# Kernel tuning notes

Hardware: AMD Instinct MI355X
Metric: run time of the kernel (lower is better)

## Reference

```python
import jax, jax.numpy as jnp
import numpy as np

STRIDE = 25
TOPK = 3
EPS = 1e-9


def setup_inputs() -> dict:
    key = jax.random.key(0)
    k1, k2, k3, k4 = jax.random.split(key, 4)
    B, N, T, P = 128, 200, 360, 400
    x = jax.random.normal(k1, (B, N, T), dtype=jnp.float32)
    # per-sample time-series lengths; min 100 so size_after_pool >= 1
    length = jax.random.randint(k2, (B,), 100, T + 1)
    # xavier_uniform with gain=1.414 as in nn.init.xavier_uniform_(.., gain=1.414)
    limit = float(np.sqrt(6.0 / (P + N)) * 1.414)
    patterns = jax.random.uniform(k3, (P, N), minval=-limit, maxval=limit, dtype=jnp.float32)
    # simple linear classifier standing in for Baselines.mlp(num_of_node)
    W_cls = jax.random.normal(k4, (N * N, 2), dtype=jnp.float32) * 0.01
    b_cls = jnp.zeros((2,), dtype=jnp.float32)
    return {"x": x, "length": length, "patterns": patterns, "W_cls": W_cls, "b_cls": b_cls}


def _forward(x, length, patterns, W_cls, b_cls):
    B, N, T = x.shape
    P = patterns.shape[0]
    # size_after_pool = floor(length / stride)  [B]
    sap = (length // STRIDE).astype(jnp.int32)
    # MRI_length_regularize (random_start=False): the scatter-mask keeps
    # t < size_after_pool*stride per sample; padded tail is exactly zero and
    # contributes 0 through maxpool+sum, so static full-T masking is equivalent.
    valid = (jnp.arange(T)[None, :] < (sap * STRIDE)[:, None]).astype(x.dtype)  # [B,T]
    frames = (x * valid[:, None, :]).transpose(0, 2, 1)  # [B,T,N]
    nf = frames / jnp.sqrt((frames ** 2).sum(-1, keepdims=True) + EPS)
    npat = patterns / jnp.sqrt((patterns ** 2).sum(-1, keepdims=True) + EPS)
    # top_select: keep top-K |entries| per pattern row
    _, topi = jax.lax.top_k(jnp.abs(npat), TOPK)  # [P,K]
    pmask = jnp.zeros((P, N), x.dtype).at[jnp.arange(P)[:, None], topi].set(1.0)
    toppattern = pmask * npat
    # scores + strided max-pool over time
    scores = jnp.einsum('btn,pn->bpt', nf, npat)  # [B,P,T]
    nwin = T // STRIDE
    pos = scores[:, :, : nwin * STRIDE].reshape(B, P, nwin, STRIDE).max(-1)  # [B,P,nwin]
    finalscore = (pos / sap[:, None, None].astype(x.dtype)).sum(-1)  # [B,P]
    # realpattern = toppattern.detach(); graphs = R^T diag(finalscore) R / (maskgraph+eps)
    realpattern = jax.lax.stop_gradient(toppattern)
    maskgraph = pmask.T @ pmask  # [N,N]
    graphs = jnp.einsum('pn,bp,pm->bnm', realpattern, finalscore, realpattern) / (maskgraph + EPS)
    out = graphs.reshape(B, -1) @ W_cls + b_cls  # [B,2]
    # Critical_ROI(normalized_patterns, toppattern)
    norm = (((1.0 - jnp.linalg.norm(toppattern, axis=-1) / jnp.linalg.norm(npat, axis=-1)) ** 2).sum() / 800.0)
    rec = jnp.zeros((1,), x.dtype)
    return out, norm, rec


def reference(x, length, patterns, W_cls, b_cls):
    return _forward(x, length, patterns, W_cls, b_cls)
```

## Files before the change

kernel.cpp:

```cpp
#include <hip/hip_runtime.h>

#define N_NODE 200
#define T_LEN 360
#define T_POOL 350
#define P_PAT 400
#define P_PAD 512
#define NWIN 14
#define STRIDE_ 25
#define KPAD 224

#define O_AH    0
#define O_POS   229376
#define O_TOPN  3899392
#define O_TOPV  3904192
#define O_NORMT 3908992

typedef unsigned short u16;
typedef __attribute__((ext_vector_type(8))) short bf16x8;
typedef __attribute__((ext_vector_type(4))) float f32x4;

#define RP 2064
#define DBS 8256
#define SQOFF 16512
#define IVOFF 18560
#define SMEM_BYTES 19072

__device__ __forceinline__ unsigned fkey(float f) {
    unsigned u = __float_as_uint(f);
    return (u & 0x80000000u) ? ~u : (u | 0x80000000u);
}
__device__ __forceinline__ u16 f2bf(float f) {
    unsigned u = __float_as_uint(f);
    unsigned r = u + 0x7FFFu + ((u >> 16) & 1u);
    return (u16)(r >> 16);
}

__global__ void k_pat(const float* __restrict__ pat, u16* __restrict__ Ah,
                      int* __restrict__ topn_w, float* __restrict__ topv_w,
                      float* __restrict__ normt, unsigned* __restrict__ pos)
{
    int p = blockIdx.x;
    int lane = threadIdx.x;
    bool pv = p < P_PAT;

    {
        int base = blockIdx.x * 64 + lane;
        #pragma unroll
        for (int i = 0; i < 28; ++i) pos[base + i * 32768] = 0u;
    }

    float sv[4], av[4];
    int nn[4];
    float ss = 0.f;
    #pragma unroll
    for (int j = 0; j < 4; ++j) {
        int n = lane + 64 * j;
        nn[j] = n;
        if (pv && n < N_NODE) { float v = pat[p * N_NODE + n]; sv[j] = v; av[j] = fabsf(v); ss += v * v; }
        else { sv[j] = 0.f; av[j] = -1.f; }
    }
    #pragma unroll
    for (int off = 32; off >= 1; off >>= 1) ss += __shfl_xor(ss, off);
    float rn = 1.0f / sqrtf(ss + 1e-9f);

    int pb = p >> 6, ii = (p >> 4) & 3, plm = p & 15;
    #pragma unroll
    for (int j = 0; j < 4; ++j) {
        int n = nn[j];
        if (n < KPAD) {
            float v = (pv && n < N_NODE) ? sv[j] * rn : 0.f;
            int s = n >> 5, c = n & 31, quad = c >> 3, e = c & 7;
            size_t idx = ((size_t)((s * 8 + pb) * 4 + ii) * 64 + quad * 16 + plm) * 8 + e;
            Ah[idx] = f2bf(v);
        }
    }
    if (!pv) return;

    int topn[3]; float topv[3];
    for (int r = 0; r < 3; ++r) {
        float bv = -2.f; int bi = 1 << 30;
        #pragma unroll
        for (int j = 0; j < 4; ++j)
            if (av[j] > bv || (av[j] == bv && nn[j] < bi)) { bv = av[j]; bi = nn[j]; }
        #pragma unroll
        for (int off = 32; off >= 1; off >>= 1) {
            float ov = __shfl_xor(bv, off); int oi = __shfl_xor(bi, off);
            if (ov > bv || (ov == bv && oi < bi)) { bv = ov; bi = oi; }
        }
        int jj = bi >> 6, src = bi & 63;
        float rawj = (jj == 0) ? sv[0] : (jj == 1) ? sv[1] : (jj == 2) ? sv[2] : sv[3];
        float raw = __shfl(rawj, src);
        topn[r] = bi; topv[r] = raw * rn;
        #pragma unroll
        for (int j = 0; j < 4; ++j) if (nn[j] == bi) av[j] = -1.f;
    }
    float fullnorm = sqrtf(ss) * rn;
    float topnorm = sqrtf(topv[0]*topv[0] + topv[1]*topv[1] + topv[2]*topv[2]);
    if (lane == 0) {
        float d = 1.0f - topnorm / fullnorm;
        normt[p] = d * d * (1.0f / 800.0f);
    }
    if (lane < 3) { topn_w[p * 3 + lane] = topn[lane]; topv_w[p * 3 + lane] = topv[lane]; }
}

__global__ __launch_bounds__(256, 3) void k_gemm(const float* __restrict__ x,
    const u16* __restrict__ AhF, const int* __restrict__ length,
    unsigned* __restrict__ pos)
{
    __shared__ __align__(16) char smem[SMEM_BYTES];
    int tid = threadIdx.x;
    int b = blockIdx.z, p0 = blockIdx.y * 128, t0 = blockIdx.x * 128;
    int lane = tid & 63, wid = tid >> 6;
    int quad = lane >> 4, lm = lane & 15;
    int wp = wid >> 1, wt = wid & 1;
    int pbq = blockIdx.y * 2 + wp;
    const float* xb = x + (size_t)b * (N_NODE * T_LEN);

    f32x4 acc[4][4];
    #pragma unroll
    for (int i = 0; i < 4; ++i)
        #pragma unroll
        for (int j = 0; j < 4; ++j) acc[i][j] = (f32x4){0.f, 0.f, 0.f, 0.f};
    float ssq0 = 0.f, ssq1 = 0.f;

    int tg = t0 + 2 * lane;
    bool tok = tg < T_LEN;
    int xfb = quad * RP + (lm & 1) * 1024 + (lm >> 1) * 16 + wt * 512;

    float2 xv[8];
    auto loadX = [&](int s) {
        int kb = s * 32 + wid * 8;
        #pragma unroll
        for (int e = 0; e < 8; ++e) {
            int k = kb + e;
            xv[e] = (tok && k < N_NODE) ? *(const float2*)(xb + k * T_LEN + tg)
                                        : make_float2(0.f, 0.f);
        }
    };
    auto cw = [&](int buf) {
        union { u16 us[8]; uint4 v; } H0, H1;
        #pragma unroll
        for (int e = 0; e < 8; ++e) {
            float f0 = xv[e].x, f1 = xv[e].y;
            ssq0 = fmaf(f0, f0, ssq0); ssq1 = fmaf(f1, f1, ssq1);
            H0.us[e] = (u16)(__float_as_uint(f0) >> 16);
            H1.us[e] = (u16)(__float_as_uint(f1) >> 16);
        }
        char* bp = smem + buf * DBS + wid * RP + lane * 16;
        *(uint4*)(bp)        = H0.v;
        *(uint4*)(bp + 1024) = H1.v;
    };

    loadX(0); cw(0);
    bf16x8 ah[4], xh[4];
    for (int s = 0; s < 7; ++s) {
        const u16* Ab = AhF + (size_t)(s * 8 + pbq) * 2048 + lane * 8;
        #pragma unroll
        for (int i = 0; i < 4; ++i) ah[i] = *(const bf16x8*)(Ab + i * 512);
        if (s < 6) loadX(s + 1);
        __syncthreads();
        const char* rb = smem + (s & 1) * DBS + xfb;
        #pragma unroll
        for (int j = 0; j < 4; ++j) xh[j] = *(const bf16x8*)(rb + j * 128);
        #pragma unroll
        for (int i = 0; i < 4; ++i)
            #pragma unroll
            for (int j = 0; j < 4; ++j)
                acc[i][j] = __builtin_amdgcn_mfma_f32_16x16x32_bf16(ah[i], xh[j], acc[i][j], 0, 0, 0);
        if (s < 6) cw((s + 1) & 1);
    }

    *(float2*)&smem[SQOFF + tid * 8] = make_float2(ssq0, ssq1);
    __syncthreads();
    int sap = length[b] / STRIDE_;
    int tvalid = sap * STRIDE_;
    if (tid < 64) {
        float a0 = 0.f, a1 = 0.f;
        #pragma unroll
        for (int w2 = 0; w2 < 4; ++w2) {
            float2 v = *(float2*)&smem[SQOFF + (w2 * 64 + tid) * 8];
            a0 += v.x; a1 += v.y;
        }
        float rs = 1.0f / (float)sap;
        int ta = t0 + 2 * tid;
        ((float*)&smem[IVOFF])[2 * tid]     = (ta     < tvalid) ? rs / sqrtf(a0 + 1e-9f) : 0.f;
        ((float*)&smem[IVOFF])[2 * tid + 1] = (ta + 1 < tvalid) ? rs / sqrtf(a1 + 1e-9f) : 0.f;
    }
    __syncthreads();
    float invv[4];
    #pragma unroll
    for (int j = 0; j < 4; ++j) invv[j] = ((float*)&smem[IVOFF])[wt * 64 + j * 16 + lm];

    float* Ss = (float*)smem;
    int wbase = t0 / STRIDE_;
    int tmax = min(t0 + 128, T_POOL);
    for (int rr = 0; rr < 4; ++rr) {
        __syncthreads();
        if (wp == (rr >> 1)) {
            #pragma unroll
            for (int i2 = 0; i2 < 2; ++i2) {
                int i = (rr & 1) * 2 + i2;
                #pragma unroll
                for (int j = 0; j < 4; ++j) {
                    int col = wt * 64 + j * 16 + lm;
                    #pragma unroll
                    for (int r = 0; r < 4; ++r)
                        Ss[(i2 * 16 + quad * 4 + r) * 132 + col] = acc[i][j][r] * invv[j];
                }
            }
        }
        __syncthreads();
        int sidx = tid & 7, pl = tid >> 3;
        int w = wbase + sidx;
        int tlo = max(w * STRIDE_, t0), thi = min(w * STRIDE_ + STRIDE_, tmax);
        if (w < NWIN && tlo < thi) {
            float m = -3.4e38f;
            for (int t = tlo; t < thi; ++t) m = fmaxf(m, Ss[pl * 132 + (t - t0)]);
            atomicMax(&pos[((size_t)b * P_PAD + p0 + rr * 32 + pl) * NWIN + w], fkey(m));
        }
    }
}

__global__ void k_out(const unsigned* __restrict__ pos, const int* __restrict__ topn_w,
                      const float* __restrict__ topv_w, const float* __restrict__ W,
                      const float* __restrict__ normt, const float* __restrict__ bcls,
                      float* __restrict__ out)
{
    __shared__ unsigned maskT[N_NODE * 13];
    __shared__ float cf0[P_PAT], cf1[P_PAT];
    __shared__ float sh[512];
    int b = blockIdx.x, tid = threadIdx.x;

    for (int i = tid; i < N_NODE * 13; i += 256) maskT[i] = 0u;
    __syncthreads();
    for (int idx = tid; idx < P_PAT * 3; idx += 256) {
        int q = idx / 3;
        int n = topn_w[idx];
        atomicOr(&maskT[n * 13 + (q >> 5)], 1u << (q & 31));
    }
    __syncthreads();

    for (int p = tid; p < P_PAT; p += 256) {
        int tn[3]; float tv[3];
        #pragma unroll
        for (int i = 0; i < 3; ++i) { tn[i] = topn_w[p * 3 + i]; tv[i] = topv_w[p * 3 + i]; }
        float c0 = 0.f, c1 = 0.f;
        #pragma unroll
        for (int i = 0; i < 3; ++i)
            #pragma unroll
            for (int j = 0; j < 3; ++j) {
                int a = tn[i], bb = tn[j];
                int mgv = 0;
                #pragma unroll
                for (int w = 0; w < 13; ++w)
                    mgv += __popc(maskT[a * 13 + w] & maskT[bb * 13 + w]);
                int nm = a * N_NODE + bb;
                float f = tv[i] * tv[j] / ((float)mgv + 1e-9f);
                c0 += f * W[nm * 2 + 0];
                c1 += f * W[nm * 2 + 1];
            }
        cf0[p] = c0; cf1[p] = c1;
    }
    __syncthreads();
    float s0 = 0.f, s1 = 0.f;
    for (int p = tid; p < P_PAT; p += 256) {
        const unsigned* pp = pos + ((size_t)b * P_PAD + p) * NWIN;
        float fs = 0.f;
        #pragma unroll
        for (int w = 0; w < NWIN; ++w) {
            unsigned k = pp[w];
            unsigned u = (k & 0x80000000u) ? (k ^ 0x80000000u) : ~k;
            fs += __uint_as_float(u);
        }
        s0 += fs * cf0[p];
        s1 += fs * cf1[p];
    }
    sh[tid] = s0; sh[256 + tid] = s1;
    __syncthreads();
    for (int o = 128; o > 0; o >>= 1) {
        if (tid < o) { sh[tid] += sh[tid + o]; sh[256 + tid] += sh[256 + tid + o]; }
        __syncthreads();
    }
    if (tid == 0) {
        out[b * 2 + 0] = sh[0]   + bcls[0];
        out[b * 2 + 1] = sh[256] + bcls[1];
    }
    if (b == 0) {
        __syncthreads();
        float ns = 0.f;
        for (int i = tid; i < P_PAT; i += 256) ns += normt[i];
        sh[tid] = ns;
        __syncthreads();
        for (int o = 128; o > 0; o >>= 1) {
            if (tid < o) sh[tid] += sh[tid + o];
            __syncthreads();
        }
        if (tid == 0) { out[256] = sh[0]; out[257] = 0.f; }
    }
}

extern "C" void kernel_launch(void* const* d_in, const int* in_sizes, int n_in,
                              void* d_out, int out_size, void* d_ws, size_t ws_size,
                              hipStream_t stream) {
    (void)in_sizes; (void)n_in; (void)out_size; (void)ws_size;
    const float* x        = (const float*)d_in[0];
    const int*   length   = (const int*)d_in[1];
    const float* patterns = (const float*)d_in[2];
    const float* Wcls     = (const float*)d_in[3];
    const float* bcls     = (const float*)d_in[4];
    float* out = (float*)d_out;
    char* ws = (char*)d_ws;

    u16*      Ah    = (u16*)(ws + O_AH);
    unsigned* pos   = (unsigned*)(ws + O_POS);
    int*      topn  = (int*)(ws + O_TOPN);
    float*    topv  = (float*)(ws + O_TOPV);
    float*    normt = (float*)(ws + O_NORMT);

    k_pat<<<P_PAD, 64, 0, stream>>>(patterns, Ah, topn, topv, normt, pos);
    k_gemm<<<dim3(3, 4, 128), 256, 0, stream>>>(x, Ah, length, pos);
    k_out<<<128, 256, 0, stream>>>(pos, topn, topv, Wcls, normt, bcls, out);
}
```

Before: 138.4 us.

## Pre-transpose x to bf16 in prep kernel and fuse output stage via last-block counter

Measured after the change: 184.9 us. +33.6%, slower.

```diff
diff --git a/kernel.cpp b/kernel.cpp
--- a/kernel.cpp
+++ b/kernel.cpp
@@ -3,6 +3,7 @@
 #define N_NODE 200
 #define T_LEN 360
 #define T_POOL 350
+#define T_PAD 384
 #define P_PAT 400
 #define P_PAD 512
 #define NWIN 14
@@ -10,20 +11,17 @@
 #define KPAD 224
 
 #define O_AH    0
-#define O_POS   229376
-#define O_TOPN  3899392
-#define O_TOPV  3904192
-#define O_NORMT 3908992
+#define O_XT    229376
+#define O_INVN  22249472
+#define O_POS   22446080
+#define O_TOPN  26116096
+#define O_TOPV  26120896
+#define O_NORMT 26125696
+#define O_CTR   26127296
 
 typedef unsigned short u16;
 typedef __attribute__((ext_vector_type(8))) short bf16x8;
 typedef __attribute__((ext_vector_type(4))) float f32x4;
-
-#define RP 2064
-#define DBS 8256
-#define SQOFF 16512
-#define IVOFF 18560
-#define SMEM_BYTES 19072
 
 __device__ __forceinline__ unsigned fkey(float f) {
     unsigned u = __float_as_uint(f);
@@ -35,163 +33,192 @@
     return (u16)(r >> 16);
 }
 
-__global__ void k_pat(const float* __restrict__ pat, u16* __restrict__ Ah,
-                      int* __restrict__ topn_w, float* __restrict__ topv_w,
-                      float* __restrict__ normt, unsigned* __restrict__ pos)
+__global__ __launch_bounds__(256) void k_prep(
+    const float* __restrict__ x, const int* __restrict__ length,
+    const float* __restrict__ pat,
+    u16* __restrict__ Ah, u16* __restrict__ XT, float* __restrict__ invn,
+    int* __restrict__ topn_w, float* __restrict__ topv_w, float* __restrict__ normt,
+    unsigned* __restrict__ pos, unsigned* __restrict__ ctr)
 {
-    int p = blockIdx.x;
-    int lane = threadIdx.x;
-    bool pv = p < P_PAT;
+    __shared__ unsigned ldsw[2176];
+    int blk = blockIdx.x, tid = threadIdx.x;
 
     {
-        int base = blockIdx.x * 64 + lane;
-        #pragma unroll
-        for (int i = 0; i < 28; ++i) pos[base + i * 32768] = 0u;
-    }
-
-    float sv[4], av[4];
-    int nn[4];
-    float ss = 0.f;
-    #pragma unroll
-    for (int j = 0; j < 4; ++j) {
-        int n = lane + 64 * j;
-        nn[j] = n;
-        if (pv && n < N_NODE) { float v = pat[p * N_NODE + n]; sv[j] = v; av[j] = fabsf(v); ss += v * v; }
-        else { sv[j] = 0.f; av[j] = -1.f; }
-    }
-    #pragma unroll
-    for (int off = 32; off >= 1; off >>= 1) ss += __shfl_xor(ss, off);
-    float rn = 1.0f / sqrtf(ss + 1e-9f);
-
-    int pb = p >> 6, ii = (p >> 4) & 3, plm = p & 15;
-    #pragma unroll
-    for (int j = 0; j < 4; ++j) {
-        int n = nn[j];
-        if (n < KPAD) {
-            float v = (pv && n < N_NODE) ? sv[j] * rn : 0.f;
-            int s = n >> 5, c = n & 31, quad = c >> 3, e = c & 7;
-            size_t idx = ((size_t)((s * 8 + pb) * 4 + ii) * 64 + quad * 16 + plm) * 8 + e;
-            Ah[idx] = f2bf(v);
-        }
-    }
-    if (!pv) return;
-
-    int topn[3]; float topv[3];
-    for (int r = 0; r < 3; ++r) {
-        float bv = -2.f; int bi = 1 << 30;
-        #pragma unroll
-        for (int j = 0; j < 4; ++j)
-            if (av[j] > bv || (av[j] == bv && nn[j] < bi)) { bv = av[j]; bi = nn[j]; }
-        #pragma unroll
-        for (int off = 32; off >= 1; off >>= 1) {
-            float ov = __shfl_xor(bv, off); int oi = __shfl_xor(bi, off);
-            if (ov > bv || (ov == bv && oi < bi)) { bv = ov; bi = oi; }
-        }
-        int jj = bi >> 6, src = bi & 63;
-        float rawj = (jj == 0) ? sv[0] : (jj == 1) ? sv[1] : (jj == 2) ? sv[2] : sv[3];
-        float raw = __shfl(rawj, src);
-        topn[r] = bi; topv[r] = raw * rn;
-        #pragma unroll
-        for (int j = 0; j < 4; ++j) if (nn[j] == bi) av[j] = -1.f;
-    }
-    float fullnorm = sqrtf(ss) * rn;
-    float topnorm = sqrtf(topv[0]*topv[0] + topv[1]*topv[1] + topv[2]*topv[2]);
-    if (lane == 0) {
-        float d = 1.0f - topnorm / fullnorm;
-        normt[p] = d * d * (1.0f / 800.0f);
-    }
-    if (lane < 3) { topn_w[p * 3 + lane] = topn[lane]; topv_w[p * 3 + lane] = topv[lane]; }
-}
-
-__global__ __launch_bounds__(256, 3) void k_gemm(const float* __restrict__ x,
-    const u16* __restrict__ AhF, const int* __restrict__ length,
-    unsigned* __restrict__ pos)
+        int base = blk * 256 + tid;
+        #pragma unroll
+        for (int i = 0; i < 7; ++i) pos[base + i * 131072] = 0u;
+    }
+    if (blk == 0 && tid < 128) ctr[tid] = 0u;
+
+    if (blk < 128) {
+        int lane = tid & 63;
+        int p = blk * 4 + (tid >> 6);
+        bool pv = p < P_PAT;
+        float sv[4], av[4];
+        int nn[4];
+        float ss = 0.f;
+        #pragma unroll
+        for (int j = 0; j < 4; ++j) {
+            int n = lane + 64 * j;
+            nn[j] = n;
+            if (pv && n < N_NODE) { float v = pat[p * N_NODE + n]; sv[j] = v; av[j] = fabsf(v); ss += v * v; }
+            else { sv[j] = 0.f; av[j] = -1.f; }
+        }
+        #pragma unroll
+        for (int off = 32; off >= 1; off >>= 1) ss += __shfl_xor(ss, off);
+        float rn = 1.0f / sqrtf(ss + 1e-9f);
+
+        int pb = p >> 6, ii = (p >> 4) & 3, plm = p & 15;
+        #pragma unroll
+        for (int j = 0; j < 4; ++j) {
+            int n = nn[j];
+            if (n < KPAD) {
+                float v = (pv && n < N_NODE) ? sv[j] * rn : 0.f;
+                int s = n >> 5, c = n & 31, quad = c >> 3, e = c & 7;
+                size_t idx = ((size_t)((s * 8 + pb) * 4 + ii) * 64 + quad * 16 + plm) * 8 + e;
+                Ah[idx] = f2bf(v);
+            }
+        }
+        if (!pv) return;
+
+        int topn[3]; float topv[3];
+        for (int r = 0; r < 3; ++r) {
+            float bv = -2.f; int bi = 1 << 30;
+            #pragma unroll
+            for (int j = 0; j < 4; ++j)
+                if (av[j] > bv || (av[j] == bv && nn[j] < bi)) { bv = av[j]; bi = nn[j]; }
+            #pragma unroll
+            for (int off = 32; off >= 1; off >>= 1) {
+                float ov = __shfl_xor(bv, off); int oi = __shfl_xor(bi, off);
+                if (ov > bv || (ov == bv && oi < bi)) { bv = ov; bi = oi; }
+            }
+            int jj = bi >> 6, src = bi & 63;
+            float rawj = (jj == 0) ? sv[0] : (jj == 1) ? sv[1] : (jj == 2) ? sv[2] : sv[3];
+            float raw = __shfl(rawj, src);
+            topn[r] = bi; topv[r] = raw * rn;
+            #pragma unroll
+            for (int j = 0; j < 4; ++j) if (nn[j] == bi) av[j] = -1.f;
+        }
+        float fullnorm = sqrtf(ss) * rn;
+        float topnorm = sqrtf(topv[0]*topv[0] + topv[1]*topv[1] + topv[2]*topv[2]);
+        if (lane == 0) {
+            float d = 1.0f - topnorm / fullnorm;
+            normt[p] = d * d * (1.0f / 800.0f);
+        }
+        if (lane < 3) { topn_w[p * 3 + lane] = topn[lane]; topv_w[p * 3 + lane] = topv[lane]; }
+        return;
+    }
+
+    int b1 = blk - 128;
+    int b = b1 / 3, ti = b1 - 3 * b;
+    int t0 = ti * 128;
+    int th = tid & 127, cg = tid >> 7;
+    int t = t0 + th;
+    bool tok = t < T_LEN;
+    const float* xb = x + (size_t)b * (N_NODE * T_LEN);
+    float ssq = 0.f;
+
+    for (int c = 0; c < 7; ++c) {
+        int k0 = c * 32;
+        #pragma unroll
+        for (int cc8 = 0; cc8 < 8; ++cc8) {
+            int cc = cg * 8 + cc8;
+            int k = k0 + cc * 2;
+            float v0 = (tok && k     < N_NODE) ? xb[k * T_LEN + t]       : 0.f;
+            float v1 = (tok && k + 1 < N_NODE) ? xb[(k + 1) * T_LEN + t] : 0.f;
+            ssq = fmaf(v0, v0, fmaf(v1, v1, ssq));
+            ldsw[th * 17 + cc] = (unsigned)f2bf(v0) | ((unsigned)f2bf(v1) << 16);
+        }
+        __syncthreads();
+        {
+            int t2 = tid >> 1, h = tid & 1;
+            unsigned w0 = ldsw[t2 * 17 + h * 4 + 0];
+            unsigned w1 = ldsw[t2 * 17 + h * 4 + 1];
+            unsigned w2 = ldsw[t2 * 17 + h * 4 + 2];
+            unsigned w3 = ldsw[t2 * 17 + h * 4 + 3];
+            uint4 val = make_uint4(w0, w1, w2, w3);
+            *(uint4*)&XT[(size_t)(b * T_PAD + t0 + t2) * KPAD + k0 + h * 8] = val;
+        }
+        __syncthreads();
+    }
+    ((float*)ldsw)[tid] = ssq;
+    __syncthreads();
+    if (tid < 128) {
+        float tot = ((float*)ldsw)[tid] + ((float*)ldsw)[tid + 128];
+        int sap = length[b] / STRIDE_;
+        int tvalid = sap * STRIDE_;
+        float iv = (t0 + tid < tvalid) ? 1.0f / (sqrtf(tot + 1e-9f) * (float)sap) : 0.f;
+        invn[b * T_PAD + t0 + tid] = iv;
+    }
+}
+
+#define LDS_SS 0
+#define LDS_MASK 0
+#define LDS_CF0 10400
+#define LDS_CF1 12000
+#define LDS_SH  13600
+#define LDS_FLAG 15648
+__global__ __launch_bounds__(256) void k_all(
+    const u16* __restrict__ Ah, const u16* __restrict__ XT,
+    const float* __restrict__ invn, unsigned* __restrict__ pos,
+    unsigned* __restrict__ ctr,
+    const int* __restrict__ topn_w, const float* __restrict__ topv_w,
+    const float* __restrict__ W, const float* __restrict__ normt,
+    const float* __restrict__ bcls, float* __restrict__ out)
 {
-    __shared__ __align__(16) char smem[SMEM_BYTES];
-    int tid = threadIdx.x;
-    int b = blockIdx.z, p0 = blockIdx.y * 128, t0 = blockIdx.x * 128;
+    __shared__ __align__(16) char smem[15664];
+    int tid = threadIdx.x, blk = blockIdx.x;
+    int xcd = blk & 7, slot = blk >> 3;
+    int g = slot / 12, r = slot - 12 * g;
+    int b = xcd + 8 * g;
+    int t0 = (r % 3) * 128;
+    int p0 = (r / 3) * 128;
     int lane = tid & 63, wid = tid >> 6;
     int quad = lane >> 4, lm = lane & 15;
     int wp = wid >> 1, wt = wid & 1;
-    int pbq = blockIdx.y * 2 + wp;
-    const float* xb = x + (size_t)b * (N_NODE * T_LEN);
+    int pbq = (p0 >> 6) + wp;
 
     f32x4 acc[4][4];
     #pragma unroll
     for (int i = 0; i < 4; ++i)
         #pragma unroll
         for (int j = 0; j < 4; ++j) acc[i][j] = (f32x4){0.f, 0.f, 0.f, 0.f};
-    float ssq0 = 0.f, ssq1 = 0.f;
-
-    int tg = t0 + 2 * lane;
-    bool tok = tg < T_LEN;
-    int xfb = quad * RP + (lm & 1) * 1024 + (lm >> 1) * 16 + wt * 512;
-
-    float2 xv[8];
-    auto loadX = [&](int s) {
-        int kb = s * 32 + wid * 8;
-        #pragma unroll
-        for (int e = 0; e < 8; ++e) {
-            int k = kb + e;
-            xv[e] = (tok && k < N_NODE) ? *(const float2*)(xb + k * T_LEN + tg)
-                                        : make_float2(0.f, 0.f);
-        }
-    };
-    auto cw = [&](int buf) {
-        union { u16 us[8]; uint4 v; } H0, H1;
-        #pragma unroll
-        for (int e = 0; e < 8; ++e) {
-            float f0 = xv[e].x, f1 = xv[e].y;
-            ssq0 = fmaf(f0, f0, ssq0); ssq1 = fmaf(f1, f1, ssq1);
-            H0.us[e] = (u16)(__float_as_uint(f0) >> 16);
-            H1.us[e] = (u16)(__float_as_uint(f1) >> 16);
-        }
-        char* bp = smem + buf * DBS + wid * RP + lane * 16;
-        *(uint4*)(bp)        = H0.v;
-        *(uint4*)(bp + 1024) = H1.v;
-    };
-
-    loadX(0); cw(0);
-    bf16x8 ah[4], xh[4];
+
+    const u16* Abase = Ah + (size_t)pbq * 2048 + lane * 8;
+    const u16* Xbase[4];
+    #pragma unroll
+    for (int j = 0; j < 4; ++j)
+        Xbase[j] = XT + (size_t)(b * T_PAD + t0 + wt * 64 + j * 16 + lm) * KPAD + quad * 8;
+
+    bf16x8 aC[4], xC[4], aN[4], xN[4];
+    #pragma unroll
+    for (int i = 0; i < 4; ++i) aC[i] = *(const bf16x8*)(Abase + i * 512);
+    #pragma unroll
+    for (int j = 0; j < 4; ++j) xC[j] = *(const bf16x8*)(Xbase[j]);
+    #pragma unroll
     for (int s = 0; s < 7; ++s) {
-        const u16* Ab = AhF + (size_t)(s * 8 + pbq) * 2048 + lane * 8;
-        #pragma unroll
-        for (int i = 0; i < 4; ++i) ah[i] = *(const bf16x8*)(Ab + i * 512);
-        if (s < 6) loadX(s + 1);
-        __syncthreads();
-        const char* rb = smem + (s & 1) * DBS + xfb;
-        #pragma unroll
-        for (int j = 0; j < 4; ++j) xh[j] = *(const bf16x8*)(rb + j * 128);
+        if (s < 6) {
+            #pragma unroll
+            for (int i = 0; i < 4; ++i) aN[i] = *(const bf16x8*)(Abase + (s + 1) * 16384 + i * 512);
+            #pragma unroll
+            for (int j = 0; j < 4; ++j) xN[j] = *(const bf16x8*)(Xbase[j] + (s + 1) * 32);
+        }
         #pragma unroll
         for (int i = 0; i < 4; ++i)
             #pragma unroll
             for (int j = 0; j < 4; ++j)
-                acc[i][j] = __builtin_amdgcn_mfma_f32_16x16x32_bf16(ah[i], xh[j], acc[i][j], 0, 0, 0);
-        if (s < 6) cw((s + 1) & 1);
-    }
-
-    *(float2*)&smem[SQOFF + tid * 8] = make_float2(ssq0, ssq1);
-    __syncthreads();
-    int sap = length[b] / STRIDE_;
-    int tvalid = sap * STRIDE_;
-    if (tid < 64) {
-        float a0 = 0.f, a1 = 0.f;
-        #pragma unroll
-        for (int w2 = 0; w2 < 4; ++w2) {
-            float2 v = *(float2*)&smem[SQOFF + (w2 * 64 + tid) * 8];
-            a0 += v.x; a1 += v.y;
-        }
-        float rs = 1.0f / (float)sap;
-        int ta = t0 + 2 * tid;
-        ((float*)&smem[IVOFF])[2 * tid]     = (ta     < tvalid) ? rs / sqrtf(a0 + 1e-9f) : 0.f;
-        ((float*)&smem[IVOFF])[2 * tid + 1] = (ta + 1 < tvalid) ? rs / sqrtf(a1 + 1e-9f) : 0.f;
-    }
-    __syncthreads();
+                acc[i][j] = __builtin_amdgcn_mfma_f32_16x16x32_bf16(aC[i], xC[j], acc[i][j], 0, 0, 0);
+        #pragma unroll
+        for (int i = 0; i < 4; ++i) aC[i] = aN[i];
+        #pragma unroll
+        for (int j = 0; j < 4; ++j) xC[j] = xN[j];
+    }
+
     float invv[4];
     #pragma unroll
-    for (int j = 0; j < 4; ++j) invv[j] = ((float*)&smem[IVOFF])[wt * 64 + j * 16 + lm];
-
-    float* Ss = (float*)smem;
+    for (int j = 0; j < 4; ++j) invv[j] = invn[b * T_PAD + t0 + wt * 64 + j * 16 + lm];
+
+    float* Ss = (float*)&smem[LDS_SS];
     int wbase = t0 / STRIDE_;
     int tmax = min(t0 + 128, T_POOL);
     for (int rr = 0; rr < 4; ++rr) {
@@ -204,8 +231,8 @@
                 for (int j = 0; j < 4; ++j) {
                     int col = wt * 64 + j * 16 + lm;
                     #pragma unroll
-                    for (int r = 0; r < 4; ++r)
-                        Ss[(i2 * 16 + quad * 4 + r) * 132 + col] = acc[i][j][r] * invv[j];
+                    for (int q = 0; q < 4; ++q)
+                        Ss[(i2 * 16 + quad * 4 + q) * 132 + col] = acc[i][j][q] * invv[j];
                 }
             }
         }
@@ -219,18 +246,24 @@
             atomicMax(&pos[((size_t)b * P_PAD + p0 + rr * 32 + pl) * NWIN + w], fkey(m));
         }
     }
-}
-
-__global__ void k_out(const unsigned* __restrict__ pos, const int* __restrict__ topn_w,
-                      const float* __restrict__ topv_w, const float* __restrict__ W,
-                      const float* __restrict__ normt, const float* __restrict__ bcls,
-                      float* __restrict__ out)
-{
-    __shared__ unsigned maskT[N_NODE * 13];
-    __shared__ float cf0[P_PAT], cf1[P_PAT];
-    __shared__ float sh[512];
-    int b = blockIdx.x, tid = threadIdx.x;
-
+
+    __syncthreads();
+    volatile int* flagp = (volatile int*)&smem[LDS_FLAG];
+    if (tid == 0) {
+        __threadfence();
+        unsigned old = atomicAdd(&ctr[b], 1u);
+        *flagp = (old == 11u) ? 1 : 0;
+    }
+    __syncthreads();
+    int flag = *flagp;
+    __syncthreads();
+    if (!flag) return;
+    __threadfence();
+
+    unsigned* maskT = (unsigned*)&smem[LDS_MASK];
+    float* cf0 = (float*)&smem[LDS_CF0];
+    float* cf1 = (float*)&smem[LDS_CF1];
+    float* sh  = (float*)&smem[LDS_SH];
     for (int i = tid; i < N_NODE * 13; i += 256) maskT[i] = 0u;
     __syncthreads();
     for (int idx = tid; idx < P_PAT * 3; idx += 256) {
@@ -239,7 +272,6 @@
         atomicOr(&maskT[n * 13 + (q >> 5)], 1u << (q & 31));
     }
     __syncthreads();
-
     for (int p = tid; p < P_PAT; p += 256) {
         int tn[3]; float tv[3];
         #pragma unroll
@@ -312,12 +344,16 @@
     char* ws = (char*)d_ws;
 
     u16*      Ah    = (u16*)(ws + O_AH);
+    u16*      XT    = (u16*)(ws + O_XT);
+    float*    invn  = (float*)(ws + O_INVN);
     unsigned* pos   = (unsigned*)(ws + O_POS);
     int*      topn  = (int*)(ws + O_TOPN);
     float*    topv  = (float*)(ws + O_TOPV);
     float*    normt = (float*)(ws + O_NORMT);
-
-    k_pat<<<P_PAD, 64, 0, stream>>>(patterns, Ah, topn, topv, normt, pos);
-    k_gemm<<<dim3(3, 4, 128), 256, 0, stream>>>(x, Ah, length, pos);
-    k_out<<<128, 256, 0, stream>>>(pos, topn, topv, Wcls, normt, bcls, out);
-}
+    unsigned* ctr   = (unsigned*)(ws + O_CTR);
+
+    k_prep<<<512, 256, 0, stream>>>(x, length, patterns, Ah, XT, invn,
+                                    topn, topv, normt, pos, ctr);
+    k_all<<<1536, 256, 0, stream>>>(Ah, XT, invn, pos, ctr,
+                                    topn, topv, Wcls, normt, bcls, out);
+}
```
